# Kernel optimization log

Hardware: AMD Instinct MI355X
Metric: run time of the kernel (lower is better)

The kernel has to match this reference:

```python
import jax, jax.numpy as jnp
import numpy as np
import math

D_EMBED, D_K, N_HEADS = 1024, 1024, 16
D_H = D_EMBED // N_HEADS          # 64
ROT_DIM = D_H // 2                # 32, RotaryEmbedding(dim=d_h//2)
B, LQ, LK = 2, 2048, 2048


def _rope_freqs(seq_len):
    # lucidrains rotary-embedding-torch: inv_freq over half of `dim`, interleave-repeated
    inv_freq = 1.0 / (10000.0 ** (jnp.arange(0, ROT_DIM, 2, dtype=jnp.float32) / ROT_DIM))
    t = jnp.arange(seq_len, dtype=jnp.float32)
    f = t[:, None] * inv_freq[None, :]          # [S, ROT_DIM/2]
    return jnp.repeat(f, 2, axis=-1)            # [S, ROT_DIM] interleaved


def _apply_rotary(x, freqs):
    # x: [B,H,S,D_H]; rotate first ROT_DIM features, pass the rest through
    x_rot, x_pass = x[..., :ROT_DIM], x[..., ROT_DIM:]
    cos, sin = jnp.cos(freqs), jnp.sin(freqs)   # [S, ROT_DIM]
    x1, x2 = x_rot[..., 0::2], x_rot[..., 1::2]
    rotated = jnp.stack((-x2, x1), axis=-1).reshape(x_rot.shape)
    return jnp.concatenate([x_rot * cos + rotated * sin, x_pass], axis=-1)


def setup_inputs() -> dict:
    key = jax.random.key(0)
    ks = jax.random.split(key, 12)
    s = 0.02
    return {
        "embed": jax.random.normal(ks[0], (B, LQ, D_EMBED), jnp.float32),
        "key": jax.random.normal(ks[1], (B, LK, D_K), jnp.float32),
        "attn_mask": jnp.ones((B, LQ, LK), dtype=bool),
        "WQ": jax.random.normal(ks[2], (D_EMBED, D_EMBED), jnp.float32) * s,
        "bQ": jnp.zeros((D_EMBED,), jnp.float32),
        "WK": jax.random.normal(ks[3], (D_K, D_EMBED), jnp.float32) * s,
        "bK": jnp.zeros((D_EMBED,), jnp.float32),
        "WV": jax.random.normal(ks[4], (D_K, D_EMBED), jnp.float32) * s,
        "bV": jnp.zeros((D_EMBED,), jnp.float32),
        "WO": jax.random.normal(ks[5], (D_EMBED, D_EMBED), jnp.float32) * s,
        "bO": jnp.zeros((D_EMBED,), jnp.float32),
    }


def reference(embed, key, attn_mask, WQ, bQ, WK, bK, WV, bV, WO, bO):
    bsz, len_q, _ = embed.shape
    len_k = key.shape[1]
    scale = 1.0 / math.sqrt(D_EMBED)  # note: module scales by 1/sqrt(d_embed)

    Q = embed @ WQ + bQ
    K = key @ WK + bK
    V = key @ WV + bV

    # [B, H, S, D_H]
    Qh = Q.reshape(bsz, len_q, N_HEADS, D_H).transpose(0, 2, 1, 3)
    Kh = K.reshape(bsz, len_k, N_HEADS, D_H).transpose(0, 2, 1, 3)
    Vh = V.reshape(bsz, len_k, N_HEADS, D_H).transpose(0, 2, 1, 3)

    Qh = _apply_rotary(Qh, _rope_freqs(len_q))
    Kh = _apply_rotary(Kh, _rope_freqs(len_k))

    attn = jnp.einsum('bhqd,bhkd->bhqk', Qh, Kh)
    attn = jnp.where(attn_mask[:, None, :, :], attn, -jnp.inf)
    attn = jax.nn.softmax(attn * scale, axis=-1)

    out = jnp.einsum('bhqk,bhkd->bhqd', attn, Vh)
    out = out.transpose(0, 2, 1, 3).reshape(bsz, len_q, D_EMBED)
    return out @ WO + bO
```

## Files before the change

kernel.cpp:

```cpp
#include <hip/hip_runtime.h>
#include <hip/hip_bf16.h>
#include <cstdint>
#include <cstddef>

typedef __bf16 bf16_t;
typedef bf16_t bf16x8 __attribute__((ext_vector_type(8)));
typedef bf16_t bf16x4 __attribute__((ext_vector_type(4)));
typedef bf16_t bf16x2 __attribute__((ext_vector_type(2)));
typedef float f32x4 __attribute__((ext_vector_type(4)));
typedef float f32x16 __attribute__((ext_vector_type(16)));
typedef unsigned int u32x4 __attribute__((ext_vector_type(4)));

namespace {
constexpr int Bv = 2, Lv = 2048, Ev = 1024, NHv = 16;
constexpr int Mv = Bv * Lv;
constexpr float SCALE_L2E = 0.03125f * 1.4426950408889634f;
}

__device__ __forceinline__ void gload_lds16(const void* g, void* l) {
  __builtin_amdgcn_global_load_lds(
      (const __attribute__((address_space(1))) unsigned int*)g,
      (__attribute__((address_space(3))) unsigned int*)l,
      16, 0, 0);
}

__global__ __launch_bounds__(256) void k_cvt2(const float* __restrict__ x0,
                                              const float* __restrict__ x1,
                                              bf16_t* __restrict__ y0,
                                              bf16_t* __restrict__ y1, int n4) {
  const float* x = blockIdx.z ? x1 : x0;
  bf16_t* y = blockIdx.z ? y1 : y0;
  int i = blockIdx.x * 256 + threadIdx.x;
  if (i < n4) {
    float4 v = reinterpret_cast<const float4*>(x)[i];
    bf16x4 o = {(bf16_t)v.x, (bf16_t)v.y, (bf16_t)v.z, (bf16_t)v.w};
    *reinterpret_cast<bf16x4*>(&y[(size_t)i * 4]) = o;
  }
}

__global__ __launch_bounds__(256) void k_twt(const float* w0, const float* w1,
                                             const float* w2, const float* w3,
                                             bf16_t* t0, bf16_t* t1,
                                             bf16_t* t2, bf16_t* t3) {
  const float* W;
  bf16_t* T;
  switch (blockIdx.z) {
    case 0: W = w0; T = t0; break;
    case 1: W = w1; T = t1; break;
    case 2: W = w2; T = t2; break;
    default: W = w3; T = t3; break;
  }
  __shared__ float tile[32][33];
  const int tx = threadIdx.x, ty = threadIdx.y;
  const int n0 = blockIdx.x * 32, k0 = blockIdx.y * 32;
#pragma unroll
  for (int i = 0; i < 4; i++) {
    int r = ty + i * 8;
    tile[r][tx] = W[(size_t)(k0 + r) * Ev + n0 + tx];
  }
  __syncthreads();
#pragma unroll
  for (int i = 0; i < 4; i++) {
    int r = ty + i * 8;
    T[(size_t)(n0 + r) * Ev + k0 + tx] = (bf16_t)tile[tx][r];
  }
}

__global__ __launch_bounds__(256) void k_trig(float2* __restrict__ tab) {
  int t = blockIdx.x * 256 + threadIdx.x;
  int i = t & 15, l = t >> 4;
  float inv = exp2f(-13.287712379549449f * (float)i * (1.0f / 16.0f));
  float s, c;
  sincosf((float)l * inv, &s, &c);
  tab[t] = make_float2(c, s);
}

__global__ __launch_bounds__(256) void k_gemm_qkv(
    const bf16_t* __restrict__ Ae, const bf16_t* __restrict__ Ak,
    const bf16_t* __restrict__ WtQ, const bf16_t* __restrict__ WtK,
    const bf16_t* __restrict__ WtV, const float* __restrict__ bQ,
    const float* __restrict__ bK, const float* __restrict__ bV,
    const float2* __restrict__ tab, bf16_t* __restrict__ Qbf,
    bf16_t* __restrict__ Kbf, bf16_t* __restrict__ Vtr) {
  constexpr int K = Ev;
  const int z = blockIdx.z;
  const bf16_t* A = (z == 0) ? Ae : Ak;
  const bf16_t* Bt = (z == 0) ? WtQ : (z == 1) ? WtK : WtV;
  const float* bias = (z == 0) ? bQ : (z == 1) ? bK : bV;

  __shared__ __align__(16) bf16_t As[128 * 32];
  __shared__ __align__(16) bf16_t Bs[128 * 32];
  const int tid = threadIdx.x;
  const int wid = tid >> 6, lane = tid & 63;
  const int bm = blockIdx.y * 128, bn = blockIdx.x * 128;
  const int wr = wid >> 1, wc = wid & 1;
  f32x4 acc[4][4] = {};
  const int srow = wid * 32 + (lane >> 2);
  const int scol = (lane & 3) * 8;
  const size_t ga0 = (size_t)(bm + srow) * K + scol;
  const size_t ga1 = (size_t)(bm + srow + 16) * K + scol;
  const size_t gb0 = (size_t)(bn + srow) * K + scol;
  const size_t gb1 = (size_t)(bn + srow + 16) * K + scol;
  bf16_t* asw = &As[wid * 1024];
  bf16_t* bsw = &Bs[wid * 1024];
  for (int k0 = 0; k0 < K; k0 += 32) {
    gload_lds16(A + ga0 + k0, asw);
    gload_lds16(A + ga1 + k0, asw + 512);
    gload_lds16(Bt + gb0 + k0, bsw);
    gload_lds16(Bt + gb1 + k0, bsw + 512);
    __syncthreads();
    bf16x8 af[4], bfr[4];
#pragma unroll
    for (int m = 0; m < 4; m++)
      af[m] = *(const bf16x8*)&As[(wr * 64 + m * 16 + (lane & 15)) * 32 + (lane >> 4) * 8];
#pragma unroll
    for (int n = 0; n < 4; n++)
      bfr[n] = *(const bf16x8*)&Bs[(wc * 64 + n * 16 + (lane & 15)) * 32 + (lane >> 4) * 8];
#pragma unroll
    for (int m = 0; m < 4; m++)
#pragma unroll
      for (int n = 0; n < 4; n++)
        acc[m][n] = __builtin_amdgcn_mfma_f32_16x16x32_bf16(af[m], bfr[n], acc[m][n], 0, 0, 0);
    __syncthreads();
  }

  const int l15 = lane & 15, g = lane >> 4;
  if (z == 2) {
#pragma unroll
    for (int n = 0; n < 4; n++) {
      const int col = bn + wc * 64 + n * 16 + l15;
      const int hh = (col >> 6) & 15;
      const int d = col & 63;
      const float bv = bias[col];
#pragma unroll
      for (int m = 0; m < 4; m++) {
        const int row0 = bm + wr * 64 + m * 16 + (g << 2);
        const int b = row0 >> 11, l0 = row0 & 2047;
        const int pq = (l0 >> 2) & 3;
        const int pq2 = ((pq & 1) << 1) | (pq >> 1);
        const int l0p = (l0 & ~12) | (pq2 << 2);
        bf16x4 ov;
#pragma unroll
        for (int r = 0; r < 4; r++) ov[r] = (bf16_t)(acc[m][n][r] + bv);
        *(bf16x4*)&Vtr[((size_t)((b * NHv + hh) * 64 + d)) * Lv + l0p] = ov;
      }
    }
    return;
  }

  bf16_t* Y = (z == 0) ? Qbf : Kbf;
  const float scale = (z == 0) ? SCALE_L2E : 1.0f;
  const float ssign = (l15 & 1) ? 1.0f : -1.0f;
#pragma unroll
  for (int n = 0; n < 4; n++) {
    const int col = bn + wc * 64 + n * 16 + l15;
    const int h = (col >> 6) & 15;
    const int d = col & 63;
    const float bv = bias[col];
    const bool dorope = (d < 32);
    const int ti = d >> 1;
#pragma unroll
    for (int m = 0; m < 4; m++) {
      const int row0 = bm + wr * 64 + m * 16 + (g << 2);
#pragma unroll
      for (int r = 0; r < 4; r++) {
        const int row = row0 + r;
        const int l = row & 2047, b = row >> 11;
        float v = acc[m][n][r] + bv;
        float p = __shfl_xor(v, 1);
        float o = v;
        if (dorope) {
          float2 cs = tab[(l << 4) + ti];
          o = v * cs.x + p * cs.y * ssign;
        }
        Y[(((size_t)(b * NHv + h)) * Lv + l) * 64 + d] = (bf16_t)(o * scale);
      }
    }
  }
}

__global__ __launch_bounds__(256) void k_gemm_bt(const bf16_t* __restrict__ A,
                                                 const bf16_t* __restrict__ Bt,
                                                 const float* __restrict__ bias,
                                                 float* __restrict__ C,
                                                 int N, int K) {
  __shared__ __align__(16) bf16_t As[128 * 32];
  __shared__ __align__(16) bf16_t Bs[128 * 32];
  const int tid = threadIdx.x;
  const int wid = tid >> 6, lane = tid & 63;
  const int bm = blockIdx.y * 128, bn = blockIdx.x * 128;
  const int wr = wid >> 1, wc = wid & 1;
  f32x4 acc[4][4] = {};
  const int srow = wid * 32 + (lane >> 2);
  const int scol = (lane & 3) * 8;
  const size_t ga0 = (size_t)(bm + srow) * K + scol;
  const size_t ga1 = (size_t)(bm + srow + 16) * K + scol;
  const size_t gb0 = (size_t)(bn + srow) * K + scol;
  const size_t gb1 = (size_t)(bn + srow + 16) * K + scol;
  bf16_t* asw = &As[wid * 1024];
  bf16_t* bsw = &Bs[wid * 1024];
  for (int k0 = 0; k0 < K; k0 += 32) {
    gload_lds16(A + ga0 + k0, asw);
    gload_lds16(A + ga1 + k0, asw + 512);
    gload_lds16(Bt + gb0 + k0, bsw);
    gload_lds16(Bt + gb1 + k0, bsw + 512);
    __syncthreads();
    bf16x8 af[4], bfr[4];
#pragma unroll
    for (int m = 0; m < 4; m++)
      af[m] = *(const bf16x8*)&As[(wr * 64 + m * 16 + (lane & 15)) * 32 + (lane >> 4) * 8];
#pragma unroll
    for (int n = 0; n < 4; n++)
      bfr[n] = *(const bf16x8*)&Bs[(wc * 64 + n * 16 + (lane & 15)) * 32 + (lane >> 4) * 8];
#pragma unroll
    for (int m = 0; m < 4; m++)
#pragma unroll
      for (int n = 0; n < 4; n++)
        acc[m][n] = __builtin_amdgcn_mfma_f32_16x16x32_bf16(af[m], bfr[n], acc[m][n], 0, 0, 0);
    __syncthreads();
  }
#pragma unroll
  for (int n = 0; n < 4; n++) {
    const int col = bn + wc * 64 + n * 16 + (lane & 15);
    const float bv = bias[col];
#pragma unroll
    for (int m = 0; m < 4; m++) {
      const int row0 = bm + wr * 64 + m * 16 + ((lane >> 4) << 2);
#pragma unroll
      for (int r = 0; r < 4; r++)
        C[(size_t)(row0 + r) * N + col] = acc[m][n][r] + bv;
    }
  }
}

__global__ void k_flag_init(int* f) { f[0] = 1; f[1] = 1; }

__global__ __launch_bounds__(256) void k_mask_and(const unsigned int* __restrict__ m,
                                                  int* __restrict__ f, int nwords) {
  int i = blockIdx.x * 256 + threadIdx.x;
  const int u8words = nwords >> 2;
  bool badA = false, badB = false;
  for (; i < nwords; i += gridDim.x * 256) {
    unsigned int v = m[i];
    badA |= (i < u8words) & (v != 0x01010101u);
    badB |= (v != 1u);
  }
  if (__any(badA) && (threadIdx.x & 63) == 0) f[0] = 0;
  if (__any(badB) && (threadIdx.x & 63) == 0) f[1] = 0;
}

__device__ __forceinline__ void flash_stage(const bf16_t* __restrict__ Kg,
                                            const bf16_t* __restrict__ Vg,
                                            bf16_t* ksb, bf16_t* vsb,
                                            int tid, int kt) {
#pragma unroll
  for (int i = 0; i < 2; i++) {
    int slot = i * 256 + tid;
    int r = slot >> 3, c = slot & 7;
    int sb = ((c * 16) ^ ((r & 7) << 4)) >> 1;
    bf16_t* dk = ksb + (size_t)(i * 256 + (tid & 192)) * 8;
    gload_lds16(Kg + (size_t)(kt * 64 + r) * 64 + sb, dk);
    bf16_t* dv = vsb + (size_t)(i * 256 + (tid & 192)) * 8;
    gload_lds16(Vg + (size_t)r * Lv + kt * 64 + sb, dv);
  }
}

__global__ __launch_bounds__(256) void k_flash32(const bf16_t* __restrict__ Qh,
                                                 const bf16_t* __restrict__ Kh,
                                                 const bf16_t* __restrict__ Vtr,
                                                 const int* __restrict__ mask,
                                                 const int* __restrict__ allflag,
                                                 bf16_t* __restrict__ Oh) {
  __shared__ __align__(16) bf16_t Ks[2][64 * 64];
  __shared__ __align__(16) bf16_t Vs[2][64 * 64];
  __shared__ float sw[4][32];
  const int tid = threadIdx.x, wid = tid >> 6, lane = tid & 63;
  const int l31 = lane & 31, hf = lane >> 5;
  const int qt = blockIdx.x, bh = blockIdx.y;
  const int b = bh >> 4, hd = bh & 15;
  const size_t base = (size_t)bh * Lv * 64;
  const bf16_t* Kg = Kh + base;
  const bf16_t* Vg = Vtr + base;
  const int allm = allflag[0] | allflag[1];
  const int q = qt * 128 + wid * 32 + l31;

  bf16x8 bq[4];
#pragma unroll
  for (int s = 0; s < 4; s++)
    bq[s] = *(const bf16x8*)&Qh[base + (size_t)q * 64 + s * 16 + hf * 8];

  const int xsw = (l31 & 7) << 4;
  int eo_[4];
#pragma unroll
  for (int s = 0; s < 4; s++) eo_[s] = (((s * 16 + hf * 8) * 2) ^ xsw) >> 1;

  float m_r = -INFINITY, l_p = 0.f;
  f32x16 o0 = {}, o1 = {};

  flash_stage(Kg, Vg, Ks[0], Vs[0], tid, 0);
  __syncthreads();
  int cur = 0;
  for (int kt = 0; kt < Lv / 64; ++kt) {
    if (kt + 1 < Lv / 64)
      flash_stage(Kg, Vg, Ks[cur ^ 1], Vs[cur ^ 1], tid, kt + 1);
    const bf16_t* KsC = Ks[cur];
    const bf16_t* VsC = Vs[cur];

    f32x16 st0 = {}, st1 = {};
    __builtin_amdgcn_s_setprio(1);
#pragma unroll
    for (int s = 0; s < 4; s++) {
      bf16x8 k0 = *(const bf16x8*)&KsC[l31 * 64 + eo_[s]];
      bf16x8 k1 = *(const bf16x8*)&KsC[(32 + l31) * 64 + eo_[s]];
      st0 = __builtin_amdgcn_mfma_f32_32x32x16_bf16(k0, bq[s], st0, 0, 0, 0);
      st1 = __builtin_amdgcn_mfma_f32_32x32x16_bf16(k1, bq[s], st1, 0, 0, 0);
    }
    __builtin_amdgcn_s_setprio(0);

    if (!allm) {
      const int* mrow = &mask[(size_t)b * Lv * Lv + (size_t)q * Lv + kt * 64];
#pragma unroll
      for (int r = 0; r < 16; r++) {
        const int kv = (r & 3) + 8 * (r >> 2) + 4 * hf;
        if (!mrow[kv]) st0[r] = -INFINITY;
        if (!mrow[32 + kv]) st1[r] = -INFINITY;
      }
    }

    float pm = st0[0];
#pragma unroll
    for (int r = 1; r < 16; r++) pm = fmaxf(pm, st0[r]);
#pragma unroll
    for (int r = 0; r < 16; r++) pm = fmaxf(pm, st1[r]);
    if (__any(pm > m_r + 8.0f)) {
      float pmf = fmaxf(pm, __shfl_xor(pm, 32));
      float mn = fmaxf(m_r, pmf);
      float alpha = exp2f(m_r - mn);
      m_r = mn;
      l_p *= alpha;
      if (!hf) sw[wid][l31] = alpha;
      asm volatile("s_waitcnt lgkmcnt(0)" ::: "memory");
      __builtin_amdgcn_sched_barrier(0);
#pragma unroll
      for (int r = 0; r < 16; r++) {
        float a = sw[wid][(r & 3) + 8 * (r >> 2) + 4 * hf];
        o0[r] *= a;
        o1[r] *= a;
      }
    }
    float ps = 0.f;
#pragma unroll
    for (int r = 0; r < 16; r++) {
      float p = exp2f(st0[r] - m_r);
      st0[r] = p;
      ps += p;
    }
#pragma unroll
    for (int r = 0; r < 16; r++) {
      float p = exp2f(st1[r] - m_r);
      st1[r] = p;
      ps += p;
    }
    l_p += ps;

    unsigned int pk0[8], pk1[8];
#pragma unroll
    for (int i = 0; i < 8; i++) {
      float a0 = st0[2 * i], a1 = st0[2 * i + 1];
      float b0 = st1[2 * i], b1 = st1[2 * i + 1];
      asm("v_cvt_pk_bf16_f32 %0, %1, %2" : "=v"(pk0[i]) : "v"(a0), "v"(a1));
      asm("v_cvt_pk_bf16_f32 %0, %1, %2" : "=v"(pk1[i]) : "v"(b0), "v"(b1));
    }

    __builtin_amdgcn_s_setprio(1);
#pragma unroll
    for (int s = 0; s < 4; s++) {
      u32x4 u;
      if (s == 0) {
        u[0] = pk0[0]; u[1] = pk0[1]; u[2] = pk0[2]; u[3] = pk0[3];
      } else if (s == 1) {
        u[0] = pk0[4]; u[1] = pk0[5]; u[2] = pk0[6]; u[3] = pk0[7];
      } else if (s == 2) {
        u[0] = pk1[0]; u[1] = pk1[1]; u[2] = pk1[2]; u[3] = pk1[3];
      } else {
        u[0] = pk1[4]; u[1] = pk1[5]; u[2] = pk1[6]; u[3] = pk1[7];
      }
      bf16x8 pa = __builtin_bit_cast(bf16x8, u);
      bf16x8 v0 = *(const bf16x8*)&VsC[l31 * 64 + eo_[s]];
      bf16x8 v1 = *(const bf16x8*)&VsC[(32 + l31) * 64 + eo_[s]];
      o0 = __builtin_amdgcn_mfma_f32_32x32x16_bf16(pa, v0, o0, 0, 0, 0);
      o1 = __builtin_amdgcn_mfma_f32_32x32x16_bf16(pa, v1, o1, 0, 0, 0);
    }
    __builtin_amdgcn_s_setprio(0);

    __syncthreads();
    cur ^= 1;
  }

  float lt = l_p + __shfl_xor(l_p, 32);
  if (!hf) sw[wid][l31] = 1.0f / lt;
  asm volatile("s_waitcnt lgkmcnt(0)" ::: "memory");
  __builtin_amdgcn_sched_barrier(0);
#pragma unroll
  for (int r = 0; r < 16; r++) {
    const int rq = (r & 3) + 8 * (r >> 2) + 4 * hf;
    float inv = sw[wid][rq];
    const int qg = qt * 128 + wid * 32 + rq;
    const size_t off = ((size_t)(b * Lv + qg)) * Ev + hd * 64;
    Oh[off + l31] = (bf16_t)(o0[r] * inv);
    Oh[off + 32 + l31] = (bf16_t)(o1[r] * inv);
  }
}

extern "C" void kernel_launch(void* const* d_in, const int* in_sizes, int n_in,
                              void* d_out, int out_size, void* d_ws, size_t ws_size,
                              hipStream_t stream) {
  const float* embed = (const float*)d_in[0];
  const float* key = (const float*)d_in[1];
  const int* mask = (const int*)d_in[2];
  const float* WQ = (const float*)d_in[3];
  const float* bQ = (const float*)d_in[4];
  const float* WK = (const float*)d_in[5];
  const float* bK = (const float*)d_in[6];
  const float* WV = (const float*)d_in[7];
  const float* bV = (const float*)d_in[8];
  const float* WO = (const float*)d_in[9];
  const float* bO = (const float*)d_in[10];
  float* out = (float*)d_out;
  char* ws = (char*)d_ws;
  const size_t MB = 1024 * 1024;

  bf16_t* Wt = (bf16_t*)(ws);
  bf16_t* Ae = (bf16_t*)(ws + 8 * MB);
  bf16_t* Ak = (bf16_t*)(ws + 16 * MB);
  bf16_t* Qbf = (bf16_t*)(ws + 40 * MB);
  bf16_t* Kbf = (bf16_t*)(ws + 48 * MB);
  bf16_t* Vtr = (bf16_t*)(ws + 56 * MB);
  bf16_t* AO = (bf16_t*)(ws + 8 * MB);
  int* flag = (int*)(ws + 64 * MB);
  float2* tab = (float2*)(ws + 65 * MB);

  {
    dim3 cg(4096, 1, 2);
    k_cvt2<<<cg, 256, 0, stream>>>(embed, key, Ae, Ak, Mv * Ev / 4);
  }
  {
    dim3 tb(32, 8), tg(32, 32, 4);
    k_twt<<<tg, tb, 0, stream>>>(WQ, WK, WV, WO, Wt, Wt + 1024 * 1024,
                                 Wt + 2 * 1024 * 1024, Wt + 3 * 1024 * 1024);
  }
  k_trig<<<128, 256, 0, stream>>>(tab);
  k_flag_init<<<1, 1, 0, stream>>>(flag);
  k_mask_and<<<2048, 256, 0, stream>>>((const unsigned int*)mask, flag,
                                       Bv * Lv * Lv);

  {
    dim3 gg(8, 32, 3);
    k_gemm_qkv<<<gg, 256, 0, stream>>>(Ae, Ak, Wt, Wt + 1024 * 1024,
                                       Wt + 2 * 1024 * 1024, bQ, bK, bV, tab,
                                       Qbf, Kbf, Vtr);
  }
  {
    dim3 fg(16, 32);
    k_flash32<<<fg, 256, 0, stream>>>(Qbf, Kbf, Vtr, mask, flag, AO);
  }
  {
    dim3 gg(8, 32);
    k_gemm_bt<<<gg, 256, 0, stream>>>(AO, Wt + 3 * 1024 * 1024, bO, out, Ev, Ev);
  }
}
```

Before: 180.1 us.

## Load V fragments directly from global memory and shrink flash blocks to two waves

The flash kernel no longer stages V tiles through LDS. Each lane now loads its V^T fragments straight from global memory into registers at the start of every key tile, and only K stays double-buffered in LDS. The block size drops from 256 to 128 threads (64 queries per block) and the grid doubles, which halves LDS use per block and should allow more blocks per CU. The cost is that the V global loads are no longer shared across waves in a block, so each V tile is fetched twice per 128 queries, and the load latency sits just before the PV MFMAs with no prefetch.

```diff
diff --git a/kernel.cpp b/kernel.cpp
--- a/kernel.cpp
+++ b/kernel.cpp
@@ -249,40 +249,35 @@
   if (__any(badB) && (threadIdx.x & 63) == 0) f[1] = 0;
 }
 
-__device__ __forceinline__ void flash_stage(const bf16_t* __restrict__ Kg,
-                                            const bf16_t* __restrict__ Vg,
-                                            bf16_t* ksb, bf16_t* vsb,
-                                            int tid, int kt) {
-#pragma unroll
-  for (int i = 0; i < 2; i++) {
-    int slot = i * 256 + tid;
+__device__ __forceinline__ void flash_stage_k(const bf16_t* __restrict__ Kg,
+                                              bf16_t* ksb, int tid, int kt) {
+#pragma unroll
+  for (int i = 0; i < 4; i++) {
+    int slot = i * 128 + tid;
     int r = slot >> 3, c = slot & 7;
     int sb = ((c * 16) ^ ((r & 7) << 4)) >> 1;
-    bf16_t* dk = ksb + (size_t)(i * 256 + (tid & 192)) * 8;
+    bf16_t* dk = ksb + (size_t)(i * 128 + (tid & 64)) * 8;
     gload_lds16(Kg + (size_t)(kt * 64 + r) * 64 + sb, dk);
-    bf16_t* dv = vsb + (size_t)(i * 256 + (tid & 192)) * 8;
-    gload_lds16(Vg + (size_t)r * Lv + kt * 64 + sb, dv);
-  }
-}
-
-__global__ __launch_bounds__(256) void k_flash32(const bf16_t* __restrict__ Qh,
+  }
+}
+
+__global__ __launch_bounds__(128) void k_flash32(const bf16_t* __restrict__ Qh,
                                                  const bf16_t* __restrict__ Kh,
                                                  const bf16_t* __restrict__ Vtr,
                                                  const int* __restrict__ mask,
                                                  const int* __restrict__ allflag,
                                                  bf16_t* __restrict__ Oh) {
   __shared__ __align__(16) bf16_t Ks[2][64 * 64];
-  __shared__ __align__(16) bf16_t Vs[2][64 * 64];
-  __shared__ float sw[4][32];
+  __shared__ float sw[2][32];
   const int tid = threadIdx.x, wid = tid >> 6, lane = tid & 63;
   const int l31 = lane & 31, hf = lane >> 5;
   const int qt = blockIdx.x, bh = blockIdx.y;
   const int b = bh >> 4, hd = bh & 15;
   const size_t base = (size_t)bh * Lv * 64;
   const bf16_t* Kg = Kh + base;
-  const bf16_t* Vg = Vtr + base;
+  const bf16_t* Vg = Vtr + base + (size_t)l31 * Lv + hf * 8;
   const int allm = allflag[0] | allflag[1];
-  const int q = qt * 128 + wid * 32 + l31;
+  const int q = qt * 64 + wid * 32 + l31;
 
   bf16x8 bq[4];
 #pragma unroll
@@ -297,14 +292,22 @@
   float m_r = -INFINITY, l_p = 0.f;
   f32x16 o0 = {}, o1 = {};
 
-  flash_stage(Kg, Vg, Ks[0], Vs[0], tid, 0);
+  flash_stage_k(Kg, Ks[0], tid, 0);
   __syncthreads();
   int cur = 0;
   for (int kt = 0; kt < Lv / 64; ++kt) {
+    bf16x8 v0[4], v1[4];
+    {
+      const bf16_t* vt0 = Vg + kt * 64;
+#pragma unroll
+      for (int s = 0; s < 4; s++) {
+        v0[s] = *(const bf16x8*)(vt0 + s * 16);
+        v1[s] = *(const bf16x8*)(vt0 + (size_t)32 * Lv + s * 16);
+      }
+    }
     if (kt + 1 < Lv / 64)
-      flash_stage(Kg, Vg, Ks[cur ^ 1], Vs[cur ^ 1], tid, kt + 1);
+      flash_stage_k(Kg, Ks[cur ^ 1], tid, kt + 1);
     const bf16_t* KsC = Ks[cur];
-    const bf16_t* VsC = Vs[cur];
 
     f32x16 st0 = {}, st1 = {};
     __builtin_amdgcn_s_setprio(1);
@@ -386,10 +389,8 @@
         u[0] = pk1[4]; u[1] = pk1[5]; u[2] = pk1[6]; u[3] = pk1[7];
       }
       bf16x8 pa = __builtin_bit_cast(bf16x8, u);
-      bf16x8 v0 = *(const bf16x8*)&VsC[l31 * 64 + eo_[s]];
-      bf16x8 v1 = *(const bf16x8*)&VsC[(32 + l31) * 64 + eo_[s]];
-      o0 = __builtin_amdgcn_mfma_f32_32x32x16_bf16(pa, v0, o0, 0, 0, 0);
-      o1 = __builtin_amdgcn_mfma_f32_32x32x16_bf16(pa, v1, o1, 0, 0, 0);
+      o0 = __builtin_amdgcn_mfma_f32_32x32x16_bf16(pa, v0[s], o0, 0, 0, 0);
+      o1 = __builtin_amdgcn_mfma_f32_32x32x16_bf16(pa, v1[s], o1, 0, 0, 0);
     }
     __builtin_amdgcn_s_setprio(0);
 
@@ -405,7 +406,7 @@
   for (int r = 0; r < 16; r++) {
     const int rq = (r & 3) + 8 * (r >> 2) + 4 * hf;
     float inv = sw[wid][rq];
-    const int qg = qt * 128 + wid * 32 + rq;
+    const int qg = qt * 64 + wid * 32 + rq;
     const size_t off = ((size_t)(b * Lv + qg)) * Ev + hd * 64;
     Oh[off + l31] = (bf16_t)(o0[r] * inv);
     Oh[off + 32 + l31] = (bf16_t)(o1[r] * inv);
@@ -461,8 +462,8 @@
                                        Qbf, Kbf, Vtr);
   }
   {
-    dim3 fg(16, 32);
-    k_flash32<<<fg, 256, 0, stream>>>(Qbf, Kbf, Vtr, mask, flag, AO);
+    dim3 fg(32, 32);
+    k_flash32<<<fg, 128, 0, stream>>>(Qbf, Kbf, Vtr, mask, flag, AO);
   }
   {
     dim3 gg(8, 32);
```

After: 189.8 us. 5.3% more time.
